# Optimization experiments

Measured on AMD Instinct MI355X. Metric: run time of the kernel, lower is better.

## Reference

```python
import jax, jax.numpy as jnp
import numpy as np

DIM = 1024
HEADS = 16
HEAD_DIM = DIM // HEADS
SCALE = 1.0 / np.sqrt(HEAD_DIM).astype(np.float32)


def setup_inputs() -> dict:
    key = jax.random.key(0)
    ks = jax.random.split(key, 5)
    B, N, C = 2, 2048, DIM
    x = jax.random.normal(ks[0], (B, N, C), dtype=jnp.float32)
    w_qkv = jax.random.normal(ks[1], (C, 3 * C), dtype=jnp.float32) * (1.0 / np.sqrt(C))
    b_qkv = jax.random.normal(ks[2], (3 * C,), dtype=jnp.float32) * 0.02
    w_proj = jax.random.normal(ks[3], (C, C), dtype=jnp.float32) * (1.0 / np.sqrt(C))
    b_proj = jax.random.normal(ks[4], (C,), dtype=jnp.float32) * 0.02
    return {"x": x, "w_qkv": w_qkv, "b_qkv": b_qkv, "w_proj": w_proj, "b_proj": b_proj}


def reference(x, w_qkv, b_qkv, w_proj, b_proj):
    B, N, C = x.shape
    H, D = HEADS, C // HEADS
    # fused QKV projection: [B,N,3C] -> [3,B,H,N,D]
    qkv = (x @ w_qkv + b_qkv).reshape(B, N, 3, H, D).transpose(2, 0, 3, 1, 4)
    q, k, v = qkv[0], qkv[1], qkv[2]
    # scores [B,H,N,N]
    scores = jnp.einsum("bhnd,bhmd->bhnm", q, k) * SCALE
    attn = jax.nn.softmax(scores, axis=-1)
    # attention output -> [B,N,C]
    y = jnp.einsum("bhnm,bhmd->bhnd", attn, v).transpose(0, 2, 1, 3).reshape(B, N, C)
    return y @ w_proj + b_proj
```

## Files before the change

### kernel.cpp

```cpp
#include <hip/hip_runtime.h>
#include <stdint.h>

typedef __attribute__((ext_vector_type(8))) short bf16x8;
typedef __attribute__((ext_vector_type(4))) float f32x4;
typedef __attribute__((ext_vector_type(4))) unsigned short us4;

#define DEV static __device__ __forceinline__

DEV unsigned short f2b(float f){
  union{float f; unsigned u;} x; x.f=f;
  unsigned r = x.u + 0x7fffu + ((x.u>>16)&1u);
  return (unsigned short)(r>>16);
}

DEV void glds16(const void* g, void* l){
  __builtin_amdgcn_global_load_lds((const __attribute__((address_space(1))) void*)g,
                                   (__attribute__((address_space(3))) void*)l, 16, 0, 0);
}

__global__ __launch_bounds__(256) void convert_k(const float* __restrict__ in,
                                                 unsigned short* __restrict__ out, int n){
  int i = (blockIdx.x*256 + threadIdx.x)*8;
  if(i >= n) return;
  f32x4 a = *(const f32x4*)(in + i);
  f32x4 b = *(const f32x4*)(in + i + 4);
  us4 o0, o1;
  o0.x=f2b(a[0]); o0.y=f2b(a[1]); o0.z=f2b(a[2]); o0.w=f2b(a[3]);
  o1.x=f2b(b[0]); o1.y=f2b(b[1]); o1.z=f2b(b[2]); o1.w=f2b(b[3]);
  *(us4*)(out + i) = o0;
  *(us4*)(out + i + 4) = o1;
}

__global__ __launch_bounds__(256) void transpose_k(const float* __restrict__ in,
                                                   unsigned short* __restrict__ out,
                                                   int ldin, int ldout){
  __shared__ __attribute__((aligned(16))) unsigned short tile[64][72];
  const int c0 = blockIdx.x*64, r0 = blockIdx.y*64;
  const int t = threadIdx.x;
  const int tr = t>>4, tc4 = (t&15)*4;
  #pragma unroll
  for(int j=0;j<4;j++){
    int r = tr + j*16;
    f32x4 v = *(const f32x4*)(in + (size_t)(r0+r)*ldin + c0 + tc4);
    tile[r][tc4+0] = f2b(v[0]);
    tile[r][tc4+1] = f2b(v[1]);
    tile[r][tc4+2] = f2b(v[2]);
    tile[r][tc4+3] = f2b(v[3]);
  }
  __syncthreads();
  #pragma unroll
  for(int j=0;j<4;j++){
    int r = tr + j*16;
    us4 v;
    v.x = tile[tc4+0][r];
    v.y = tile[tc4+1][r];
    v.z = tile[tc4+2][r];
    v.w = tile[tc4+3][r];
    *(us4*)(out + (size_t)(c0+r)*ldout + r0 + tc4) = v;
  }
}

#define BK 64

DEV void gemm_core_128(const unsigned short* __restrict__ A,
                       const unsigned short* __restrict__ Bt,
                       int K, int rowA0, int rowB0,
                       unsigned short* As, unsigned short* Bs, f32x4 acc[4][4])
{
  const int t = threadIdx.x;
  const int lane = t & 63;
  const int wid  = t >> 6;
  const int wm = wid >> 1, wn = wid & 1;
  const f32x4 Z = {0.f,0.f,0.f,0.f};

  #pragma unroll
  for(int m=0;m<4;m++)
    #pragma unroll
    for(int n=0;n<4;n++) acc[m][n] = Z;

  for(int kt=0; kt<K; kt+=BK){
    __syncthreads();
    #pragma unroll
    for(int j=0;j<4;j++){
      int idx = t + 256*j;
      int row = idx >> 3;
      int ls  = (idx & 7) ^ (row & 7);
      glds16(A + (size_t)(rowA0 + row)*K + kt + ls*8, As + (size_t)(wid*64 + 256*j)*8);
    }
    #pragma unroll
    for(int j=0;j<4;j++){
      int idx = t + 256*j;
      int row = idx >> 3;
      int ls  = (idx & 7) ^ (row & 7);
      glds16(Bt + (size_t)(rowB0 + row)*K + kt + ls*8, Bs + (size_t)(wid*64 + 256*j)*8);
    }
    __syncthreads();
    #pragma unroll
    for(int ks=0; ks<2; ks++){
      bf16x8 af[4], bfr[4];
      #pragma unroll
      for(int m=0;m<4;m++){
        int row = wm*64 + m*16 + (lane&15);
        int sl  = (ks*4 + (lane>>4)) ^ (row&7);
        af[m] = *(const bf16x8*)(As + row*64 + sl*8);
      }
      #pragma unroll
      for(int n=0;n<4;n++){
        int row = wn*64 + n*16 + (lane&15);
        int sl  = (ks*4 + (lane>>4)) ^ (row&7);
        bfr[n] = *(const bf16x8*)(Bs + row*64 + sl*8);
      }
      #pragma unroll
      for(int m=0;m<4;m++)
        #pragma unroll
        for(int n=0;n<4;n++)
          acc[m][n] = __builtin_amdgcn_mfma_f32_16x16x32_bf16(af[m], bfr[n], acc[m][n], 0, 0, 0);
    }
  }
}

__global__ __launch_bounds__(256) void gemm_qkv(const unsigned short* __restrict__ xb,
                                                const unsigned short* __restrict__ Wt,
                                                const float* __restrict__ bqkv,
                                                unsigned short* __restrict__ q,
                                                unsigned short* __restrict__ k,
                                                unsigned short* __restrict__ vt)
{
  __shared__ __attribute__((aligned(16))) unsigned short SMEM[2*128*BK];
  unsigned short* As = SMEM;
  unsigned short* Bs = SMEM + 128*BK;
  f32x4 acc[4][4];
  const int bm = blockIdx.x, bn = blockIdx.y;
  gemm_core_128(xb, Wt, 1024, bm*128, bn*128, As, Bs, acc);
  __syncthreads();

  const int t = threadIdx.x, lane = t&63, wid = t>>6, wm = wid>>1, wn = wid&1;
  const int col0 = bn*128 + wn*64;
  const int three = col0 >> 10;
  const int h = (col0>>6)&15;
  const int row0 = bm*128 + wm*64;
  const int bb = row0 >> 11, nn0 = row0 & 2047;
  const size_t bh = (size_t)(bb*16 + h);

  if(three < 2){
    unsigned short* dst = (three==0) ? q : k;
    #pragma unroll
    for(int m=0;m<4;m++)
      #pragma unroll
      for(int n=0;n<4;n++){
        int d = (col0 & 63) + n*16 + (lane&15);
        float bias = bqkv[col0 + n*16 + (lane&15)];
        #pragma unroll
        for(int r=0;r<4;r++){
          int nn = nn0 + m*16 + (lane>>4)*4 + r;
          dst[(bh*2048 + nn)*64 + d] = f2b(acc[m][n][r] + bias);
        }
      }
  } else {
    unsigned short* ep = SMEM + wid*4096;
    #pragma unroll
    for(int n=0;n<4;n++){
      int dl = n*16 + (lane&15);
      float bias = bqkv[col0 + dl];
      #pragma unroll
      for(int m=0;m<4;m++){
        int nl = m*16 + (lane>>4)*4;
        unsigned w0, w1;
        float a0 = acc[m][n][0] + bias, a1 = acc[m][n][1] + bias;
        float a2 = acc[m][n][2] + bias, a3 = acc[m][n][3] + bias;
        asm("v_cvt_pk_bf16_f32 %0, %1, %2" : "=v"(w0) : "v"(a0), "v"(a1));
        asm("v_cvt_pk_bf16_f32 %0, %1, %2" : "=v"(w1) : "v"(a2), "v"(a3));
        *(unsigned*)(ep + dl*64 + nl)     = w0;
        *(unsigned*)(ep + dl*64 + nl + 2) = w1;
      }
    }
    #pragma unroll
    for(int p=0;p<16;p++){
      int dl = p*4 + (lane>>4);
      us4 vv = *(const us4*)(ep + dl*64 + (lane&15)*4);
      *(us4*)(vt + (bh*64 + dl)*2048 + nn0 + (lane&15)*4) = vv;
    }
  }
}

__global__ __launch_bounds__(256) void gemm_proj(const unsigned short* __restrict__ y,
                                                 const unsigned short* __restrict__ Wt,
                                                 const float* __restrict__ bp,
                                                 float* __restrict__ out)
{
  __shared__ __attribute__((aligned(16))) unsigned short As[128*BK];
  __shared__ __attribute__((aligned(16))) unsigned short Bs[128*BK];
  f32x4 acc[4][4];
  const int bm = blockIdx.x, bn = blockIdx.y;
  gemm_core_128(y, Wt, 1024, bm*128, bn*128, As, Bs, acc);

  const int t = threadIdx.x, lane = t&63, wid = t>>6, wm = wid>>1, wn = wid&1;
  #pragma unroll
  for(int m=0;m<4;m++)
    #pragma unroll
    for(int n=0;n<4;n++){
      int col = bn*128 + wn*64 + n*16 + (lane&15);
      float bias = bp[col];
      #pragma unroll
      for(int r=0;r<4;r++){
        int row = bm*128 + wm*64 + m*16 + (lane>>4)*4 + r;
        out[(size_t)row*1024 + col] = acc[m][n][r] + bias;
      }
    }
}

__global__ __launch_bounds__(256, 4) void attn_k(const unsigned short* __restrict__ qg,
                                                 const unsigned short* __restrict__ kg,
                                                 const unsigned short* __restrict__ vtg,
                                                 unsigned short* __restrict__ y)
{
  __shared__ __attribute__((aligned(16))) unsigned short Ks[2][64*64];
  __shared__ __attribute__((aligned(16))) unsigned short VT[2][64*64];
  __shared__ __attribute__((aligned(16))) unsigned short Ps[4][16*64];

  const int bh = blockIdx.x;
  const int qt = blockIdx.y;
  const int b  = bh >> 4, h = bh & 15;
  const unsigned short* qh = qg  + (size_t)bh*2048*64;
  const unsigned short* kh = kg  + (size_t)bh*2048*64;
  const unsigned short* vh = vtg + (size_t)bh*64*2048;

  const int t = threadIdx.x, lane = t & 63, wid = t >> 6;
  const int q0 = qt*64 + wid*16;
  const int lq = lane & 15;
  const int lh = lane >> 4;
  const float C1 = 0.18033688011112042f;

  bf16x8 aq[2];
  #pragma unroll
  for(int ks=0;ks<2;ks++){
    int row = q0 + lq;
    aq[ks] = *(const bf16x8*)(qh + (size_t)row*64 + ks*32 + lh*8);
  }

  const f32x4 Z = {0.f,0.f,0.f,0.f};
  f32x4 accT[4];
  #pragma unroll
  for(int df=0;df<4;df++) accT[df] = Z;
  float lpart = 0.f;

  #pragma unroll
  for(int j=0;j<2;j++){
    int idx = t + 256*j;
    int row = idx >> 3;
    int ls  = (idx & 7) ^ (row & 7);
    glds16(kh + (size_t)row*64 + ls*8, &Ks[0][0] + (wid*64 + 256*j)*8);
    glds16(vh + (size_t)row*2048 + ls*8, &VT[0][0] + (wid*64 + 256*j)*8);
  }
  __syncthreads();

  for(int it=0; it<32; ++it){
    const int cur = it & 1, nxt = cur ^ 1;
    if(it < 31){
      int kvn = (it+1)*64;
      #pragma unroll
      for(int j=0;j<2;j++){
        int idx = t + 256*j;
        int row = idx >> 3;
        int ls  = (idx & 7) ^ (row & 7);
        glds16(kh + (size_t)(kvn+row)*64 + ls*8, &Ks[nxt][0] + (wid*64 + 256*j)*8);
        glds16(vh + (size_t)row*2048 + kvn + ls*8, &VT[nxt][0] + (wid*64 + 256*j)*8);
      }
    }

    f32x4 st[4];
    #pragma unroll
    for(int nc=0;nc<4;nc++) st[nc] = Z;
    __builtin_amdgcn_s_setprio(1);
    #pragma unroll
    for(int ks=0;ks<2;ks++){
      bf16x8 bk[4];
      #pragma unroll
      for(int nc=0;nc<4;nc++){
        int kvr = nc*16 + lq;
        int sl  = (ks*4 + lh) ^ (kvr&7);
        bk[nc] = *(const bf16x8*)(&Ks[cur][0] + kvr*64 + sl*8);
      }
      #pragma unroll
      for(int nc=0;nc<4;nc++)
        st[nc] = __builtin_amdgcn_mfma_f32_16x16x32_bf16(bk[nc], aq[ks], st[nc], 0,0,0);
    }
    __builtin_amdgcn_s_setprio(0);

    {
      float rs = 0.f;
      unsigned short* pr = &Ps[wid][0] + lq*64;
      #pragma unroll
      for(int nc=0;nc<4;nc++){
        float p0 = __builtin_amdgcn_exp2f(st[nc][0]*C1);
        float p1 = __builtin_amdgcn_exp2f(st[nc][1]*C1);
        float p2 = __builtin_amdgcn_exp2f(st[nc][2]*C1);
        float p3 = __builtin_amdgcn_exp2f(st[nc][3]*C1);
        rs += (p0+p1)+(p2+p3);
        unsigned w0, w1;
        asm("v_cvt_pk_bf16_f32 %0, %1, %2" : "=v"(w0) : "v"(p0), "v"(p1));
        asm("v_cvt_pk_bf16_f32 %0, %1, %2" : "=v"(w1) : "v"(p2), "v"(p3));
        int g    = 2*nc + (lh>>1);
        int phys = g ^ (lane&7);
        unsigned* dst = (unsigned*)(pr + phys*8 + (lh&1)*4);
        dst[0] = w0; dst[1] = w1;
      }
      lpart += rs;
    }

    __builtin_amdgcn_s_setprio(1);
    #pragma unroll
    for(int ks=0;ks<2;ks++){
      bf16x8 bv[4], pa;
      #pragma unroll
      for(int df=0;df<4;df++){
        int dr = df*16 + lq;
        int sl = (ks*4 + lh) ^ (dr&7);
        bv[df] = *(const bf16x8*)(&VT[cur][0] + dr*64 + sl*8);
      }
      {
        int g    = 4*ks + lh;
        int phys = g ^ (lane&7);
        pa = *(const bf16x8*)(&Ps[wid][0] + lq*64 + phys*8);
      }
      #pragma unroll
      for(int df=0;df<4;df++)
        accT[df] = __builtin_amdgcn_mfma_f32_16x16x32_bf16(bv[df], pa, accT[df], 0,0,0);
    }
    __builtin_amdgcn_s_setprio(0);

    __syncthreads();
  }

  float ls = lpart;
  ls += __shfl_xor(ls, 16, 64);
  ls += __shfl_xor(ls, 32, 64);
  float rl = 1.0f / ls;
  int row = q0 + lq;
  #pragma unroll
  for(int df=0;df<4;df++){
    us4 o;
    o.x = f2b(accT[df][0] * rl);
    o.y = f2b(accT[df][1] * rl);
    o.z = f2b(accT[df][2] * rl);
    o.w = f2b(accT[df][3] * rl);
    *(us4*)(y + ((size_t)b*2048 + row)*1024 + h*64 + df*16 + lh*4) = o;
  }
}

extern "C" void kernel_launch(void* const* d_in, const int* in_sizes, int n_in,
                              void* d_out, int out_size, void* d_ws, size_t ws_size,
                              hipStream_t stream) {
  const float* x     = (const float*)d_in[0];
  const float* wqkv  = (const float*)d_in[1];
  const float* bqkv  = (const float*)d_in[2];
  const float* wproj = (const float*)d_in[3];
  const float* bproj = (const float*)d_in[4];
  float* out = (float*)d_out;

  char* ws = (char*)d_ws;
  unsigned short* Wt1 = (unsigned short*)ws;  ws += (size_t)3072*1024*2;
  unsigned short* Wt2 = (unsigned short*)ws;  ws += (size_t)1024*1024*2;
  unsigned short* xb  = (unsigned short*)ws;  ws += (size_t)2*2048*1024*2;
  unsigned short* q   = (unsigned short*)ws;  ws += (size_t)2*16*2048*64*2;
  unsigned short* k   = (unsigned short*)ws;  ws += (size_t)2*16*2048*64*2;
  unsigned short* vt  = (unsigned short*)ws;  ws += (size_t)2*16*2048*64*2;
  unsigned short* y   = (unsigned short*)ws;  ws += (size_t)2*2048*1024*2;

  convert_k  <<<2048, 256, 0, stream>>>(x, xb, 2*2048*1024);
  transpose_k<<<dim3(48,16), 256, 0, stream>>>(wqkv,  Wt1, 3072, 1024);
  transpose_k<<<dim3(16,16), 256, 0, stream>>>(wproj, Wt2, 1024, 1024);
  gemm_qkv  <<<dim3(32,24), 256, 0, stream>>>(xb, Wt1, bqkv, q, k, vt);
  attn_k    <<<dim3(32,32), 256, 0, stream>>>(q, k, vt, y);
  gemm_proj <<<dim3(32, 8), 256, 0, stream>>>(y, Wt2, bproj, out);
}
```

Measured before the change: 134.4 us.

## Give each attention wave two query sub-tiles to reuse K/V fragments

The attention kernel now runs 128 threads (2 waves) per block, with each wave handling 32 query rows as two 16-row sub-tiles instead of one. Each K and V^T fragment read from LDS feeds twice as many MFMAs, which halves LDS read traffic per unit of compute. The K/V staging loop is rewritten so half as many threads load the same tile. In exchange each wave holds more registers, there are fewer waves per block to hide latency, and the block-per-CU occupancy hint is dropped.

```diff
diff --git a/kernel.cpp b/kernel.cpp
--- a/kernel.cpp
+++ b/kernel.cpp
@@ -209,14 +209,14 @@
     }
 }
 
-__global__ __launch_bounds__(256, 4) void attn_k(const unsigned short* __restrict__ qg,
-                                                 const unsigned short* __restrict__ kg,
-                                                 const unsigned short* __restrict__ vtg,
-                                                 unsigned short* __restrict__ y)
+__global__ __launch_bounds__(128) void attn_k(const unsigned short* __restrict__ qg,
+                                              const unsigned short* __restrict__ kg,
+                                              const unsigned short* __restrict__ vtg,
+                                              unsigned short* __restrict__ y)
 {
   __shared__ __attribute__((aligned(16))) unsigned short Ks[2][64*64];
   __shared__ __attribute__((aligned(16))) unsigned short VT[2][64*64];
-  __shared__ __attribute__((aligned(16))) unsigned short Ps[4][16*64];
+  __shared__ __attribute__((aligned(16))) unsigned short Ps[2][2][16*64];
 
   const int bh = blockIdx.x;
   const int qt = blockIdx.y;
@@ -226,51 +226,55 @@
   const unsigned short* vh = vtg + (size_t)bh*64*2048;
 
   const int t = threadIdx.x, lane = t & 63, wid = t >> 6;
-  const int q0 = qt*64 + wid*16;
+  const int q0 = qt*64 + wid*32;
   const int lq = lane & 15;
   const int lh = lane >> 4;
   const float C1 = 0.18033688011112042f;
 
-  bf16x8 aq[2];
-  #pragma unroll
-  for(int ks=0;ks<2;ks++){
-    int row = q0 + lq;
-    aq[ks] = *(const bf16x8*)(qh + (size_t)row*64 + ks*32 + lh*8);
-  }
+  bf16x8 aq[2][2];
+  #pragma unroll
+  for(int m=0;m<2;m++)
+    #pragma unroll
+    for(int ks=0;ks<2;ks++){
+      int row = q0 + m*16 + lq;
+      aq[m][ks] = *(const bf16x8*)(qh + (size_t)row*64 + ks*32 + lh*8);
+    }
 
   const f32x4 Z = {0.f,0.f,0.f,0.f};
-  f32x4 accT[4];
-  #pragma unroll
-  for(int df=0;df<4;df++) accT[df] = Z;
-  float lpart = 0.f;
-
-  #pragma unroll
-  for(int j=0;j<2;j++){
-    int idx = t + 256*j;
-    int row = idx >> 3;
-    int ls  = (idx & 7) ^ (row & 7);
-    glds16(kh + (size_t)row*64 + ls*8, &Ks[0][0] + (wid*64 + 256*j)*8);
-    glds16(vh + (size_t)row*2048 + ls*8, &VT[0][0] + (wid*64 + 256*j)*8);
-  }
+  f32x4 accT[2][4];
+  #pragma unroll
+  for(int m=0;m<2;m++)
+    #pragma unroll
+    for(int df=0;df<4;df++) accT[m][df] = Z;
+  float lpart[2] = {0.f, 0.f};
+
+#define STAGE(SRC, DSTBASE, ROWSTRIDE, COLOFF) do{                             \
+    _Pragma("unroll")                                                          \
+    for(int j=0;j<4;j++){                                                      \
+      int idx = t + 128*j;                                                     \
+      int row = idx >> 3;                                                      \
+      int ls  = (idx & 7) ^ (row & 7);                                         \
+      glds16((SRC) + (size_t)row*(ROWSTRIDE) + (COLOFF) + ls*8,                \
+             (DSTBASE) + (size_t)(wid*64 + 128*j)*8);                          \
+    }}while(0)
+
+  STAGE(kh, &Ks[0][0], 64, 0);
+  STAGE(vh, &VT[0][0], 2048, 0);
   __syncthreads();
 
   for(int it=0; it<32; ++it){
     const int cur = it & 1, nxt = cur ^ 1;
     if(it < 31){
       int kvn = (it+1)*64;
-      #pragma unroll
-      for(int j=0;j<2;j++){
-        int idx = t + 256*j;
-        int row = idx >> 3;
-        int ls  = (idx & 7) ^ (row & 7);
-        glds16(kh + (size_t)(kvn+row)*64 + ls*8, &Ks[nxt][0] + (wid*64 + 256*j)*8);
-        glds16(vh + (size_t)row*2048 + kvn + ls*8, &VT[nxt][0] + (wid*64 + 256*j)*8);
-      }
-    }
-
-    f32x4 st[4];
-    #pragma unroll
-    for(int nc=0;nc<4;nc++) st[nc] = Z;
+      STAGE(kh + (size_t)kvn*64, &Ks[nxt][0], 64, 0);
+      STAGE(vh, &VT[nxt][0], 2048, kvn);
+    }
+
+    f32x4 st[2][4];
+    #pragma unroll
+    for(int m=0;m<2;m++)
+      #pragma unroll
+      for(int nc=0;nc<4;nc++) st[m][nc] = Z;
     __builtin_amdgcn_s_setprio(1);
     #pragma unroll
     for(int ks=0;ks<2;ks++){
@@ -282,20 +286,23 @@
         bk[nc] = *(const bf16x8*)(&Ks[cur][0] + kvr*64 + sl*8);
       }
       #pragma unroll
-      for(int nc=0;nc<4;nc++)
-        st[nc] = __builtin_amdgcn_mfma_f32_16x16x32_bf16(bk[nc], aq[ks], st[nc], 0,0,0);
+      for(int m=0;m<2;m++)
+        #pragma unroll
+        for(int nc=0;nc<4;nc++)
+          st[m][nc] = __builtin_amdgcn_mfma_f32_16x16x32_bf16(bk[nc], aq[m][ks], st[m][nc], 0,0,0);
     }
     __builtin_amdgcn_s_setprio(0);
 
-    {
+    #pragma unroll
+    for(int m=0;m<2;m++){
       float rs = 0.f;
-      unsigned short* pr = &Ps[wid][0] + lq*64;
+      unsigned short* pr = &Ps[wid][m][0] + lq*64;
       #pragma unroll
       for(int nc=0;nc<4;nc++){
-        float p0 = __builtin_amdgcn_exp2f(st[nc][0]*C1);
-        float p1 = __builtin_amdgcn_exp2f(st[nc][1]*C1);
-        float p2 = __builtin_amdgcn_exp2f(st[nc][2]*C1);
-        float p3 = __builtin_amdgcn_exp2f(st[nc][3]*C1);
+        float p0 = __builtin_amdgcn_exp2f(st[m][nc][0]*C1);
+        float p1 = __builtin_amdgcn_exp2f(st[m][nc][1]*C1);
+        float p2 = __builtin_amdgcn_exp2f(st[m][nc][2]*C1);
+        float p3 = __builtin_amdgcn_exp2f(st[m][nc][3]*C1);
         rs += (p0+p1)+(p2+p3);
         unsigned w0, w1;
         asm("v_cvt_pk_bf16_f32 %0, %1, %2" : "=v"(w0) : "v"(p0), "v"(p1));
@@ -305,46 +312,52 @@
         unsigned* dst = (unsigned*)(pr + phys*8 + (lh&1)*4);
         dst[0] = w0; dst[1] = w1;
       }
-      lpart += rs;
+      lpart[m] += rs;
     }
 
     __builtin_amdgcn_s_setprio(1);
     #pragma unroll
     for(int ks=0;ks<2;ks++){
-      bf16x8 bv[4], pa;
+      bf16x8 bv[4];
       #pragma unroll
       for(int df=0;df<4;df++){
         int dr = df*16 + lq;
         int sl = (ks*4 + lh) ^ (dr&7);
         bv[df] = *(const bf16x8*)(&VT[cur][0] + dr*64 + sl*8);
       }
-      {
+      #pragma unroll
+      for(int m=0;m<2;m++){
+        bf16x8 pa;
         int g    = 4*ks + lh;
         int phys = g ^ (lane&7);
-        pa = *(const bf16x8*)(&Ps[wid][0] + lq*64 + phys*8);
-      }
-      #pragma unroll
-      for(int df=0;df<4;df++)
-        accT[df] = __builtin_amdgcn_mfma_f32_16x16x32_bf16(bv[df], pa, accT[df], 0,0,0);
+        pa = *(const bf16x8*)(&Ps[wid][m][0] + lq*64 + phys*8);
+        #pragma unroll
+        for(int df=0;df<4;df++)
+          accT[m][df] = __builtin_amdgcn_mfma_f32_16x16x32_bf16(bv[df], pa, accT[m][df], 0,0,0);
+      }
     }
     __builtin_amdgcn_s_setprio(0);
 
     __syncthreads();
   }
-
-  float ls = lpart;
-  ls += __shfl_xor(ls, 16, 64);
-  ls += __shfl_xor(ls, 32, 64);
-  float rl = 1.0f / ls;
-  int row = q0 + lq;
-  #pragma unroll
-  for(int df=0;df<4;df++){
-    us4 o;
-    o.x = f2b(accT[df][0] * rl);
-    o.y = f2b(accT[df][1] * rl);
-    o.z = f2b(accT[df][2] * rl);
-    o.w = f2b(accT[df][3] * rl);
-    *(us4*)(y + ((size_t)b*2048 + row)*1024 + h*64 + df*16 + lh*4) = o;
+#undef STAGE
+
+  #pragma unroll
+  for(int m=0;m<2;m++){
+    float ls = lpart[m];
+    ls += __shfl_xor(ls, 16, 64);
+    ls += __shfl_xor(ls, 32, 64);
+    float rl = 1.0f / ls;
+    int row = q0 + m*16 + lq;
+    #pragma unroll
+    for(int df=0;df<4;df++){
+      us4 o;
+      o.x = f2b(accT[m][df][0] * rl);
+      o.y = f2b(accT[m][df][1] * rl);
+      o.z = f2b(accT[m][df][2] * rl);
+      o.w = f2b(accT[m][df][3] * rl);
+      *(us4*)(y + ((size_t)b*2048 + row)*1024 + h*64 + df*16 + lh*4) = o;
+    }
   }
 }
 
@@ -371,6 +384,6 @@
   transpose_k<<<dim3(48,16), 256, 0, stream>>>(wqkv,  Wt1, 3072, 1024);
   transpose_k<<<dim3(16,16), 256, 0, stream>>>(wproj, Wt2, 1024, 1024);
   gemm_qkv  <<<dim3(32,24), 256, 0, stream>>>(xb, Wt1, bqkv, q, k, vt);
-  attn_k    <<<dim3(32,32), 256, 0, stream>>>(q, k, vt, y);
+  attn_k    <<<dim3(32,32), 128, 0, stream>>>(q, k, vt, y);
   gemm_proj <<<dim3(32, 8), 256, 0, stream>>>(y, Wt2, bproj, out);
 }
```

Measured after the change: 139.0 us. 1.03x slower.
